# Performance work log

Measured on AMD Instinct MI355X. Metric: run time of the kernel, lower is better.

The kernel has to match this reference:

```python
import jax, jax.numpy as jnp
import numpy as np

GROUP = 64      # quantization group size along the K (in_features) dim
QMAX = 7.0      # symmetric signed int4 range [-7, 7]


def fake_quant_w4a4(t):
    """Per-group symmetric int4 fake-quantization along last dim (STE-friendly).

    t: [..., K] with K % GROUP == 0. Emulates nunchaku's quantize_w4a4
    numerics: scale = max|group| / 7, q = clip(round(t/scale)) * scale.
    """
    shp = t.shape
    g = t.reshape(shp[:-1] + (shp[-1] // GROUP, GROUP))
    scale = jnp.maximum(jnp.max(jnp.abs(g), axis=-1, keepdims=True) / QMAX, 1e-8)
    q = jnp.clip(jnp.round(g / scale), -QMAX, QMAX) * scale
    # straight-through estimator so gradients flow through the quant branch
    q = g + jax.lax.stop_gradient(q - g)
    return q.reshape(shp)


def setup_inputs() -> dict:
    key = jax.random.key(0)
    k0, k1, k2, k3, k4, k5 = jax.random.split(key, 6)
    B, K, N, R = 8192, 2048, 2048, 32  # tokens, in_features, out_features, rank
    x = jax.random.normal(k0, (B, K), jnp.float32)
    residual_weight = jax.random.normal(k1, (N, K), jnp.float32) * 0.02
    lora_down = jax.random.normal(k2, (K, R), jnp.float32) * 0.02
    lora_up = jax.random.normal(k3, (N, R), jnp.float32) * 0.02
    smooth = jax.random.uniform(k4, (K,), jnp.float32, minval=0.5, maxval=2.0)
    bias = jax.random.normal(k5, (N,), jnp.float32) * 0.01
    return {"x": x, "residual_weight": residual_weight, "lora_down": lora_down,
            "lora_up": lora_up, "smooth": smooth, "bias": bias}


def reference(x, residual_weight, lora_down, lora_up, smooth, bias):
    """SVDQuant forward: W4A4 GEMM on the residual weight fused with an
    FP low-rank (SVD) correction and per-channel smoothing.

    y = Q4(x*smooth) @ Q4(W_res).T + (x*smooth) @ lora_down @ lora_up.T + bias
    """
    x_s = x * smooth                                   # [B, K] smoothed activations
    y_lr = (x_s @ lora_down) @ lora_up.T               # [B, R] -> [B, N] low-rank branch
    y_q = fake_quant_w4a4(x_s) @ fake_quant_w4a4(residual_weight).T  # int4xint4 branch
    return y_q + y_lr + bias
```

## Files before the change

### kernel.cpp

```cpp
#include <hip/hip_runtime.h>
#include <stdint.h>


typedef __attribute__((ext_vector_type(8))) short short8;
typedef __attribute__((ext_vector_type(8))) unsigned short ushort8;
typedef __attribute__((ext_vector_type(4))) unsigned short ushort4v;
typedef __attribute__((ext_vector_type(4))) float floatx4;

#define M_TOK 8192
#define K_IN  2048
#define N_OUT 2048
#define RANK  32
#define KC    2112
#define XS_STRIDE 2056

__device__ __forceinline__ unsigned short f2bf(float f) {
  unsigned int u = __float_as_uint(f);
  u += 0x7fff + ((u >> 16) & 1);
  return (unsigned short)(u >> 16);
}

__device__ __forceinline__ void quant8(const float* v, unsigned short* q) {
  float amax = 0.f;
#pragma unroll
  for (int i = 0; i < 8; ++i) amax = fmaxf(amax, fabsf(v[i]));
  amax = fmaxf(amax, __shfl_xor(amax, 1, 64));
  amax = fmaxf(amax, __shfl_xor(amax, 2, 64));
  amax = fmaxf(amax, __shfl_xor(amax, 4, 64));
  float scale = fmaxf(amax / 7.0f, 1e-8f);
#pragma unroll
  for (int i = 0; i < 8; ++i) {
    float qq = rintf(v[i] / scale);
    qq = fminf(fmaxf(qq, -7.f), 7.f);
    q[i] = f2bf(qq * scale);
  }
}

__global__ __launch_bounds__(256) void prep_kernel(const float* __restrict__ x,
                                                   const float* __restrict__ smooth,
                                                   const float* __restrict__ wgt,
                                                   const float* __restrict__ ld,
                                                   const float* __restrict__ lup,
                                                   unsigned short* __restrict__ Xcat,
                                                   unsigned short* __restrict__ Wcat) {
  __shared__ unsigned short xs[16 * XS_STRIDE];
  __shared__ float red[4][16][32];
  int tid = threadIdx.x;

  if (blockIdx.x >= 512) {
    int row = blockIdx.x - 512;
    const float4* wr = (const float4*)(wgt + (size_t)row * K_IN);
    float4 a0 = wr[tid * 2], a1 = wr[tid * 2 + 1];
    float v[8] = {a0.x, a0.y, a0.z, a0.w, a1.x, a1.y, a1.z, a1.w};
    ushort8 q;
    quant8(v, (unsigned short*)&q);
    *(ushort8*)(Wcat + (size_t)row * KC + tid * 8) = q;
    if (tid < 32)      Wcat[(size_t)row * KC + 2048 + tid] = f2bf(lup[row * RANK + tid]);
    else if (tid < 64) Wcat[(size_t)row * KC + 2048 + tid] = 0;
    return;
  }

  int rowbase = blockIdx.x * 16;
  int w = tid >> 6, lane = tid & 63, quad = lane >> 4, l16 = lane & 15;

  const float4* sr = (const float4*)smooth;
  float4 s0 = sr[tid * 2], s1 = sr[tid * 2 + 1];
#pragma unroll 2
  for (int r = 0; r < 16; ++r) {
    const float4* xr = (const float4*)(x + (size_t)(rowbase + r) * K_IN);
    float4 a0 = xr[tid * 2], a1 = xr[tid * 2 + 1];
    float v[8] = {a0.x * s0.x, a0.y * s0.y, a0.z * s0.z, a0.w * s0.w,
                  a1.x * s1.x, a1.y * s1.y, a1.z * s1.z, a1.w * s1.w};
    ushort8 q;
    quant8(v, (unsigned short*)&q);
    *(ushort8*)(Xcat + (size_t)(rowbase + r) * KC + tid * 8) = q;
    ushort8 sb;
#pragma unroll
    for (int t = 0; t < 8; ++t) sb[t] = f2bf(v[t]);
    *(ushort8*)(xs + r * XS_STRIDE + tid * 8) = sb;
  }
  *(unsigned int*)(Xcat + (size_t)(rowbase + (tid >> 4)) * KC + 2080 + (tid & 15) * 2) = 0u;
  __syncthreads();

  floatx4 acc[2];
  acc[0] = (floatx4)0.f;
  acc[1] = (floatx4)0.f;
  int kbase = w * 512;
#pragma unroll 2
  for (int it = 0; it < 16; ++it) {
    int k = kbase + it * 32 + quad * 8;
    short8 af = *(const short8*)(xs + l16 * XS_STRIDE + k);
    short8 b0, b1;
#pragma unroll
    for (int j = 0; j < 8; ++j) {
      b0[j] = (short)f2bf(ld[(size_t)(k + j) * RANK + l16]);
      b1[j] = (short)f2bf(ld[(size_t)(k + j) * RANK + 16 + l16]);
    }
    acc[0] = __builtin_amdgcn_mfma_f32_16x16x32_bf16(af, b0, acc[0], 0, 0, 0);
    acc[1] = __builtin_amdgcn_mfma_f32_16x16x32_bf16(af, b1, acc[1], 0, 0, 0);
  }
#pragma unroll
  for (int nt = 0; nt < 2; ++nt)
#pragma unroll
    for (int r = 0; r < 4; ++r)
      red[w][quad * 4 + r][nt * 16 + l16] = acc[nt][r];
  __syncthreads();
  if (tid < 128) {
    int rl = tid >> 3, seg = tid & 7;
    ushort4v o;
#pragma unroll
    for (int j = 0; j < 4; ++j) {
      int c = seg * 4 + j;
      float s = red[0][rl][c] + red[1][rl][c] + red[2][rl][c] + red[3][rl][c];
      o[j] = f2bf(s);
    }
    *(ushort4v*)(Xcat + (size_t)(rowbase + rl) * KC + 2048 + seg * 4) = o;
  }
}

__device__ __forceinline__ void gld_lds16(const unsigned short* g, unsigned short* l) {
  __builtin_amdgcn_global_load_lds(
      (const __attribute__((address_space(1))) unsigned int*)g,
      (__attribute__((address_space(3))) unsigned int*)l, 16, 0, 0);
}

__global__ __launch_bounds__(256) void gemm_kernel(const unsigned short* __restrict__ Xcat,
                                                   const unsigned short* __restrict__ Wcat,
                                                   const float* __restrict__ bias,
                                                   float* __restrict__ out) {
  __shared__ unsigned short smem[16384];
  unsigned short* smemA = smem;
  unsigned short* smemB = smem + 8192;
  int tid = threadIdx.x;
  int w = tid >> 6, lane = tid & 63, quad = lane >> 4, l16 = lane & 15;
  int wm = w >> 1, wn = w & 1;

  int bid = blockIdx.x;
  int g = bid >> 6, r = bid & 63;
  int bN = (r >> 2) * 128;
  int bM = (g * 4 + (r & 3)) * 128;

  int srow = tid >> 3;
  int cs = (tid & 7) ^ (srow & 7);
  const unsigned short* Ag = Xcat + (size_t)(bM + srow) * KC + cs * 8;
  const unsigned short* Bg = Wcat + (size_t)(bN + srow) * KC + cs * 8;

  int c0 = (quad ^ (l16 & 7)) * 8;
  int c1 = ((4 + quad) ^ (l16 & 7)) * 8;
  int arow[4], brow[4];
#pragma unroll
  for (int mt = 0; mt < 4; ++mt) arow[mt] = (wm * 64 + mt * 16 + l16) * 64;
#pragma unroll
  for (int nt = 0; nt < 4; ++nt) brow[nt] = (wn * 64 + nt * 16 + l16) * 64;

  floatx4 acc[4][4];
#pragma unroll
  for (int mt = 0; mt < 4; ++mt)
#pragma unroll
    for (int nt = 0; nt < 4; ++nt) acc[mt][nt] = (floatx4)0.f;

  for (int kt = 0; kt < 33; ++kt) {
    int k0 = kt * 64;
#pragma unroll
    for (int rd = 0; rd < 4; ++rd) {
      gld_lds16(Ag + (size_t)rd * 32 * KC + k0, smemA + rd * 2048 + w * 512);
      gld_lds16(Bg + (size_t)rd * 32 * KC + k0, smemB + rd * 2048 + w * 512);
    }
    __syncthreads();

    short8 af[4][2], bf[4][2];
#pragma unroll
    for (int mt = 0; mt < 4; ++mt) {
      af[mt][0] = *(const short8*)(smemA + arow[mt] + c0);
      af[mt][1] = *(const short8*)(smemA + arow[mt] + c1);
    }
#pragma unroll
    for (int nt = 0; nt < 4; ++nt) {
      bf[nt][0] = *(const short8*)(smemB + brow[nt] + c0);
      bf[nt][1] = *(const short8*)(smemB + brow[nt] + c1);
    }
#pragma unroll
    for (int kb = 0; kb < 2; ++kb)
#pragma unroll
      for (int mt = 0; mt < 4; ++mt)
#pragma unroll
        for (int nt = 0; nt < 4; ++nt)
          acc[mt][nt] = __builtin_amdgcn_mfma_f32_16x16x32_bf16(af[mt][kb], bf[nt][kb],
                                                                acc[mt][nt], 0, 0, 0);
    __syncthreads();
  }

#pragma unroll
  for (int nt = 0; nt < 4; ++nt) {
    int col = bN + wn * 64 + nt * 16 + l16;
    float bv = bias[col];
#pragma unroll
    for (int mt = 0; mt < 4; ++mt) {
      int row = bM + wm * 64 + mt * 16 + quad * 4;
#pragma unroll
      for (int r2 = 0; r2 < 4; ++r2)
        out[(size_t)(row + r2) * N_OUT + col] = acc[mt][nt][r2] + bv;
    }
  }
}

extern "C" void kernel_launch(void* const* d_in, const int* in_sizes, int n_in,
                              void* d_out, int out_size, void* d_ws, size_t ws_size,
                              hipStream_t stream) {
  const float* x      = (const float*)d_in[0];
  const float* wgt    = (const float*)d_in[1];
  const float* ld     = (const float*)d_in[2];
  const float* lup    = (const float*)d_in[3];
  const float* smooth = (const float*)d_in[4];
  const float* bias   = (const float*)d_in[5];
  float* out = (float*)d_out;

  unsigned short* Xcat = (unsigned short*)d_ws;
  unsigned short* Wcat = Xcat + (size_t)M_TOK * KC;

  hipLaunchKernelGGL(prep_kernel, dim3(512 + N_OUT), dim3(256), 0, stream,
                     x, smooth, wgt, ld, lup, Xcat, Wcat);
  hipLaunchKernelGGL(gemm_kernel, dim3((N_OUT / 128) * (M_TOK / 128)), dim3(256), 0, stream,
                     Xcat, Wcat, bias, out);
}
```

Before: 229.9 us.

## Rewrite GEMM with 256x256 tiles, triple-buffered LDS pipeline, pre-transposed lora_down

The GEMM moves to 512-thread blocks computing 256x256 tiles with a K step of 32. A three-stage LDS ring buffer is filled by async global_load_lds, and vmcnt waits replace full syncs so loads overlap MFMA, with setprio raised around the MFMA block. The concatenated K dimension shrinks from 2112 to 2080, dropping the zero padding. A small new kernel pre-transposes lora_down to bf16 so the prep kernel can load vector fragments instead of strided scalar reads. The bigger tile and triple buffer raise register and LDS use and lower occupancy.

```diff
diff --git a/kernel.cpp b/kernel.cpp
--- a/kernel.cpp
+++ b/kernel.cpp
@@ -11,7 +11,8 @@
 #define K_IN  2048
 #define N_OUT 2048
 #define RANK  32
-#define KC    2112
+#define KC    2080
+#define NKT   65
 #define XS_STRIDE 2056
 
 __device__ __forceinline__ unsigned short f2bf(float f) {
@@ -36,10 +37,19 @@
   }
 }
 
+__global__ __launch_bounds__(256) void ldt_kernel(const float* __restrict__ ld,
+                                                  unsigned short* __restrict__ ldT) {
+  int t = threadIdx.x, b = blockIdx.x;
+  int r = t & 31, kk = b * 64 + (t >> 5);
+#pragma unroll
+  for (int i = 0; i < 8; ++i)
+    ldT[r * 2048 + kk + i * 8] = f2bf(ld[(size_t)(kk + i * 8) * RANK + r]);
+}
+
 __global__ __launch_bounds__(256) void prep_kernel(const float* __restrict__ x,
                                                    const float* __restrict__ smooth,
                                                    const float* __restrict__ wgt,
-                                                   const float* __restrict__ ld,
+                                                   const unsigned short* __restrict__ ldT,
                                                    const float* __restrict__ lup,
                                                    unsigned short* __restrict__ Xcat,
                                                    unsigned short* __restrict__ Wcat) {
@@ -55,8 +65,7 @@
     ushort8 q;
     quant8(v, (unsigned short*)&q);
     *(ushort8*)(Wcat + (size_t)row * KC + tid * 8) = q;
-    if (tid < 32)      Wcat[(size_t)row * KC + 2048 + tid] = f2bf(lup[row * RANK + tid]);
-    else if (tid < 64) Wcat[(size_t)row * KC + 2048 + tid] = 0;
+    if (tid < 32) Wcat[(size_t)row * KC + 2048 + tid] = f2bf(lup[row * RANK + tid]);
     return;
   }
 
@@ -79,7 +88,6 @@
     for (int t = 0; t < 8; ++t) sb[t] = f2bf(v[t]);
     *(ushort8*)(xs + r * XS_STRIDE + tid * 8) = sb;
   }
-  *(unsigned int*)(Xcat + (size_t)(rowbase + (tid >> 4)) * KC + 2080 + (tid & 15) * 2) = 0u;
   __syncthreads();
 
   floatx4 acc[2];
@@ -90,12 +98,8 @@
   for (int it = 0; it < 16; ++it) {
     int k = kbase + it * 32 + quad * 8;
     short8 af = *(const short8*)(xs + l16 * XS_STRIDE + k);
-    short8 b0, b1;
-#pragma unroll
-    for (int j = 0; j < 8; ++j) {
-      b0[j] = (short)f2bf(ld[(size_t)(k + j) * RANK + l16]);
-      b1[j] = (short)f2bf(ld[(size_t)(k + j) * RANK + 16 + l16]);
-    }
+    short8 b0 = *(const short8*)(ldT + (size_t)l16 * 2048 + k);
+    short8 b1 = *(const short8*)(ldT + (size_t)(16 + l16) * 2048 + k);
     acc[0] = __builtin_amdgcn_mfma_f32_16x16x32_bf16(af, b0, acc[0], 0, 0, 0);
     acc[1] = __builtin_amdgcn_mfma_f32_16x16x32_bf16(af, b1, acc[1], 0, 0, 0);
   }
@@ -124,79 +128,86 @@
       (__attribute__((address_space(3))) unsigned int*)l, 16, 0, 0);
 }
 
-__global__ __launch_bounds__(256) void gemm_kernel(const unsigned short* __restrict__ Xcat,
+__global__ __launch_bounds__(512) void gemm_kernel(const unsigned short* __restrict__ Xcat,
                                                    const unsigned short* __restrict__ Wcat,
                                                    const float* __restrict__ bias,
                                                    float* __restrict__ out) {
-  __shared__ unsigned short smem[16384];
-  unsigned short* smemA = smem;
-  unsigned short* smemB = smem + 8192;
+  __shared__ unsigned short smem[49152];
   int tid = threadIdx.x;
   int w = tid >> 6, lane = tid & 63, quad = lane >> 4, l16 = lane & 15;
-  int wm = w >> 1, wn = w & 1;
+  int wm = w >> 2, wn = w & 3;
 
   int bid = blockIdx.x;
-  int g = bid >> 6, r = bid & 63;
-  int bN = (r >> 2) * 128;
-  int bM = (g * 4 + (r & 3)) * 128;
-
-  int srow = tid >> 3;
-  int cs = (tid & 7) ^ (srow & 7);
-  const unsigned short* Ag = Xcat + (size_t)(bM + srow) * KC + cs * 8;
-  const unsigned short* Bg = Wcat + (size_t)(bN + srow) * KC + cs * 8;
-
-  int c0 = (quad ^ (l16 & 7)) * 8;
-  int c1 = ((4 + quad) ^ (l16 & 7)) * 8;
-  int arow[4], brow[4];
-#pragma unroll
-  for (int mt = 0; mt < 4; ++mt) arow[mt] = (wm * 64 + mt * 16 + l16) * 64;
-#pragma unroll
-  for (int nt = 0; nt < 4; ++nt) brow[nt] = (wn * 64 + nt * 16 + l16) * 64;
-
-  floatx4 acc[4][4];
-#pragma unroll
-  for (int mt = 0; mt < 4; ++mt)
+  int wg = (bid & 7) * 32 + (bid >> 3);
+  int bM = (wg >> 3) * 256;
+  int bN = (wg & 7) * 256;
+
+  int rowA = tid >> 2;
+  int csrc = (tid & 3) ^ ((tid >> 3) & 3);
+  const unsigned short* Ag = Xcat + (size_t)(bM + rowA) * KC + csrc * 8;
+  const unsigned short* Bg = Wcat + (size_t)(bN + rowA) * KC + csrc * 8;
+  int ldsA = w * 512;
+  int ldsB = 8192 + w * 512;
+
+#define STAGE(k0, cbuf)                                                      \
+  do {                                                                       \
+    gld_lds16(Ag + (k0),            smem + (cbuf) + ldsA);                   \
+    gld_lds16(Ag + 128 * KC + (k0), smem + (cbuf) + 4096 + ldsA);            \
+    gld_lds16(Bg + (k0),            smem + (cbuf) + ldsB);                   \
+    gld_lds16(Bg + 128 * KC + (k0), smem + (cbuf) + 4096 + ldsB);            \
+  } while (0)
+
+  int cx = (quad ^ ((l16 >> 1) & 3)) * 8;
+  int aoff = (wm * 128 + l16) * 32 + cx;
+  int boff = 8192 + (wn * 64 + l16) * 32 + cx;
+
+  floatx4 acc[8][4];
+#pragma unroll
+  for (int mt = 0; mt < 8; ++mt)
 #pragma unroll
     for (int nt = 0; nt < 4; ++nt) acc[mt][nt] = (floatx4)0.f;
 
-  for (int kt = 0; kt < 33; ++kt) {
-    int k0 = kt * 64;
-#pragma unroll
-    for (int rd = 0; rd < 4; ++rd) {
-      gld_lds16(Ag + (size_t)rd * 32 * KC + k0, smemA + rd * 2048 + w * 512);
-      gld_lds16(Bg + (size_t)rd * 32 * KC + k0, smemB + rd * 2048 + w * 512);
-    }
-    __syncthreads();
-
-    short8 af[4][2], bf[4][2];
-#pragma unroll
-    for (int mt = 0; mt < 4; ++mt) {
-      af[mt][0] = *(const short8*)(smemA + arow[mt] + c0);
-      af[mt][1] = *(const short8*)(smemA + arow[mt] + c1);
-    }
-#pragma unroll
-    for (int nt = 0; nt < 4; ++nt) {
-      bf[nt][0] = *(const short8*)(smemB + brow[nt] + c0);
-      bf[nt][1] = *(const short8*)(smemB + brow[nt] + c1);
-    }
-#pragma unroll
-    for (int kb = 0; kb < 2; ++kb)
-#pragma unroll
-      for (int mt = 0; mt < 4; ++mt)
-#pragma unroll
-        for (int nt = 0; nt < 4; ++nt)
-          acc[mt][nt] = __builtin_amdgcn_mfma_f32_16x16x32_bf16(af[mt][kb], bf[nt][kb],
-                                                                acc[mt][nt], 0, 0, 0);
-    __syncthreads();
-  }
+  int c0 = 0, c1 = 16384, c2 = 32768;
+
+  STAGE(0, c0);
+  STAGE(32, c1);
+  asm volatile("s_waitcnt vmcnt(4)" ::: "memory");
+  __builtin_amdgcn_s_barrier();
+
+  for (int t = 0; t < NKT; ++t) {
+    if (t + 2 < NKT) STAGE((t + 2) * 32, c2);
+
+    short8 a[8], b[4];
+#pragma unroll
+    for (int mt = 0; mt < 8; ++mt) a[mt] = *(const short8*)(smem + c0 + aoff + mt * 512);
+#pragma unroll
+    for (int nt = 0; nt < 4; ++nt) b[nt] = *(const short8*)(smem + c0 + boff + nt * 512);
+
+    __builtin_amdgcn_s_setprio(1);
+#pragma unroll
+    for (int mt = 0; mt < 8; ++mt)
+#pragma unroll
+      for (int nt = 0; nt < 4; ++nt)
+        acc[mt][nt] = __builtin_amdgcn_mfma_f32_16x16x32_bf16(a[mt], b[nt],
+                                                              acc[mt][nt], 0, 0, 0);
+    __builtin_amdgcn_s_setprio(0);
+
+    if (t < NKT - 2)
+      asm volatile("s_waitcnt vmcnt(4)" ::: "memory");
+    else
+      asm volatile("s_waitcnt vmcnt(0)" ::: "memory");
+    __builtin_amdgcn_s_barrier();
+    int tmp = c0; c0 = c1; c1 = c2; c2 = tmp;
+  }
+#undef STAGE
 
 #pragma unroll
   for (int nt = 0; nt < 4; ++nt) {
     int col = bN + wn * 64 + nt * 16 + l16;
     float bv = bias[col];
 #pragma unroll
-    for (int mt = 0; mt < 4; ++mt) {
-      int row = bM + wm * 64 + mt * 16 + quad * 4;
+    for (int mt = 0; mt < 8; ++mt) {
+      int row = bM + wm * 128 + mt * 16 + quad * 4;
 #pragma unroll
       for (int r2 = 0; r2 < 4; ++r2)
         out[(size_t)(row + r2) * N_OUT + col] = acc[mt][nt][r2] + bv;
@@ -217,9 +228,11 @@
 
   unsigned short* Xcat = (unsigned short*)d_ws;
   unsigned short* Wcat = Xcat + (size_t)M_TOK * KC;
-
+  unsigned short* ldT  = Wcat + (size_t)N_OUT * KC;
+
+  hipLaunchKernelGGL(ldt_kernel, dim3(K_IN / 64), dim3(256), 0, stream, ld, ldT);
   hipLaunchKernelGGL(prep_kernel, dim3(512 + N_OUT), dim3(256), 0, stream,
-                     x, smooth, wgt, ld, lup, Xcat, Wcat);
-  hipLaunchKernelGGL(gemm_kernel, dim3((N_OUT / 128) * (M_TOK / 128)), dim3(256), 0, stream,
+                     x, smooth, wgt, ldT, lup, Xcat, Wcat);
+  hipLaunchKernelGGL(gemm_kernel, dim3((M_TOK / 256) * (N_OUT / 256)), dim3(512), 0, stream,
                      Xcat, Wcat, bias, out);
 }
```

Measured after the change: 214.4 us. 6.8% less time.
